# Performance work log

Hardware: AMD Instinct MI355X
Metric: run time of the kernel (lower is better)

## Reference

```python
import jax, jax.numpy as jnp
import numpy as np

B, S, D, H = 2, 2048, 2048, 16
HD = D // H  # 128 head dim


def setup_inputs() -> dict:
    key = jax.random.key(0)
    k1, k2, k3 = jax.random.split(key, 3)
    x = jax.random.normal(k1, (B, S, D), dtype=jnp.float32)
    w_qkv = jax.random.normal(k2, (3 * D, D), dtype=jnp.float32) * 0.02
    w_out = jax.random.normal(k3, (D, D), dtype=jnp.float32) * 0.02
    # complex-like RoPE table: freqs_cis[s, j] = exp(i * s * theta^{-2j/hd})
    theta = 10000.0
    inv_freq = 1.0 / (theta ** (jnp.arange(0, HD, 2, dtype=jnp.float32) / HD))  # [HD/2]
    t = jnp.arange(S, dtype=jnp.float32)
    freqs = jnp.outer(t, inv_freq)  # [S, HD/2]
    return {"x": x, "w_qkv": w_qkv, "w_out": w_out,
            "freqs_cos": jnp.cos(freqs), "freqs_sin": jnp.sin(freqs)}


def _apply_rope(t, cos, sin):
    # t: [b, s, h, hd]; adjacent pairs treated as complex (real, imag)
    b, s, h, hd = t.shape
    tr = t.reshape(b, s, h, hd // 2, 2)
    re, im = tr[..., 0], tr[..., 1]
    c = cos[None, :, None, :]  # [1, s, 1, hd/2]
    sn = sin[None, :, None, :]
    out_re = re * c - im * sn
    out_im = re * sn + im * c
    return jnp.stack([out_re, out_im], axis=-1).reshape(b, s, h, hd)


def reference(x, w_qkv, w_out, freqs_cos, freqs_sin):
    b, s, d = x.shape
    qkv = x @ w_qkv.T  # [b, s, 3d]
    q, k, v = jnp.split(qkv, 3, axis=-1)
    q = q.reshape(b, s, H, HD)
    k = k.reshape(b, s, H, HD)
    v = v.reshape(b, s, H, HD)
    q = _apply_rope(q, freqs_cos, freqs_sin)
    k = _apply_rope(k, freqs_cos, freqs_sin)
    # causal SDPA
    scale = 1.0 / jnp.sqrt(jnp.asarray(HD, dtype=x.dtype))
    scores = jnp.einsum("bqhd,bkhd->bhqk", q, k) * scale  # [b, h, s, s]
    causal = jnp.tril(jnp.ones((s, s), dtype=bool))
    scores = jnp.where(causal[None, None], scores, jnp.finfo(scores.dtype).min)
    attn = jax.nn.softmax(scores, axis=-1)
    out = jnp.einsum("bhqk,bkhd->bqhd", attn, v).reshape(b, s, d)
    return out @ w_out.T
```

## Files before the change

### kernel.cpp

```cpp
#include <hip/hip_runtime.h>
#include <hip/hip_bf16.h>
#include <stdint.h>

#define S_ 2048
#define D_ 2048
#define H_ 16
#define HD_ 128

typedef __bf16 bf16x8 __attribute__((ext_vector_type(8)));
typedef float f32x4 __attribute__((ext_vector_type(4)));
typedef unsigned short ushort_t;
typedef ushort_t us4 __attribute__((ext_vector_type(4)));

__device__ __forceinline__ float bf2f(ushort_t u) {
  union { float f; uint32_t i; } x; x.i = ((uint32_t)u) << 16; return x.f;
}
__device__ __forceinline__ ushort_t f2bf(float f) {
  union { float f; uint32_t i; } x; x.f = f;
  uint32_t r = x.i + 0x7fffu + ((x.i >> 16) & 1u);
  return (ushort_t)(r >> 16);
}

__device__ __forceinline__ void async_copy16(const void* g, void* l) {
  __builtin_amdgcn_global_load_lds(
      (const __attribute__((address_space(1))) unsigned int*)g,
      (__attribute__((address_space(3))) unsigned int*)l, 16, 0, 0);
}

__device__ __forceinline__ void store_val(float* p, float v) { *p = v; }
__device__ __forceinline__ void store_val(ushort_t* p, float v) { *p = f2bf(v); }

__global__ __launch_bounds__(256) void cvt_f32_bf16(const float* __restrict__ in,
                                                    ushort_t* __restrict__ out,
                                                    int n4) {
  int i = blockIdx.x * 256 + threadIdx.x;
  if (i >= n4) return;
  const float4 v = ((const float4*)in)[i];
  us4 o;
  o.x = f2bf(v.x); o.y = f2bf(v.y); o.z = f2bf(v.z); o.w = f2bf(v.w);
  ((us4*)out)[i] = o;
}

__device__ __forceinline__ void stage_half(const ushort_t* __restrict__ g, int K,
                                           ushort_t* l, int wave, int srow,
                                           int clog) {
#pragma unroll
  for (int i = 0; i < 2; ++i)
    async_copy16(g + (size_t)(i * 64 + srow) * K + clog * 8,
                 l + wave * 512 + i * 4096);
}

#define MFMA_BF16(a, b, c) __builtin_amdgcn_mfma_f32_16x16x32_bf16(a, b, c, 0, 0, 0)

template <typename OutT>
__global__ __launch_bounds__(512, 2) void gemm_bt128_256(const ushort_t* __restrict__ A,
                                                         const ushort_t* __restrict__ Bm,
                                                         OutT* __restrict__ C,
                                                         int M, int N, int K) {
  __shared__ __align__(16) ushort_t As[2][128 * 64];
  __shared__ __align__(16) ushort_t Bs[2][256 * 64];
  const int tid = threadIdx.x;
  const int wave = tid >> 6, lane = tid & 63;
  const int quad = lane >> 4, l16 = lane & 15;
  const int bm = blockIdx.y * 128, bn = blockIdx.x * 256;
  const int wm = (wave >> 2) * 64;
  const int wn = (wave & 3) * 64;
  const int srow = tid >> 3;
  const int clog = (tid & 7) ^ (srow & 7);
  const int ck0 = (quad ^ (l16 & 7)) * 8;
  const int ck1 = ((4 + quad) ^ (l16 & 7)) * 8;

  const ushort_t* gA = A + (size_t)bm * K;
  const ushort_t* gB = Bm + (size_t)bn * K;
  const int NT = K >> 6;

  f32x4 acc[4][4] = {};

  const ushort_t* ArowE = &As[0][0] + (wm + l16) * 64;
  const ushort_t* BrowE = &Bs[0][0] + (wn + l16) * 64;
  const ushort_t* ArowO = &As[1][0] + (wm + l16) * 64;
  const ushort_t* BrowO = &Bs[1][0] + (wn + l16) * 64;

  stage_half(gA, K, &As[0][0], wave, srow, clog);
  stage_half(gB, K, &Bs[0][0], wave, srow, clog);
  stage_half(gB + (size_t)128 * K, K, &Bs[0][8192], wave, srow, clog);
  stage_half(gB + 64, K, &Bs[1][0], wave, srow, clog);
  stage_half(gB + (size_t)128 * K + 64, K, &Bs[1][8192], wave, srow, clog);
  asm volatile("s_waitcnt vmcnt(4)" ::: "memory");
  __builtin_amdgcn_sched_barrier(0);
  __builtin_amdgcn_s_barrier();

  for (int ii = 0; ii < (NT >> 1); ++ii) {
    const int t = 2 * ii;
    const int t2 = (t + 2 < NT) ? t + 2 : NT - 1;
    const int t3 = (t + 3 < NT) ? t + 3 : NT - 1;
    const size_t k1 = (size_t)(t + 1) * 64;
    const size_t k2 = (size_t)t2 * 64;
    const size_t k3 = (size_t)t3 * 64;

    bf16x8 a4[4][2], b01[2][2], b23[2][2];

#pragma unroll
    for (int mi = 0; mi < 2; ++mi) {
      a4[mi][0] = *(const bf16x8*)(ArowE + mi * 1024 + ck0);
      a4[mi][1] = *(const bf16x8*)(ArowE + mi * 1024 + ck1);
    }
#pragma unroll
    for (int ni = 0; ni < 2; ++ni) {
      b01[ni][0] = *(const bf16x8*)(BrowE + ni * 1024 + ck0);
      b01[ni][1] = *(const bf16x8*)(BrowE + ni * 1024 + ck1);
    }
    stage_half(gA + k1, K, &As[1][0], wave, srow, clog);
    __builtin_amdgcn_s_barrier();
    __builtin_amdgcn_s_setprio(1);
#pragma unroll
    for (int ks = 0; ks < 2; ++ks)
#pragma unroll
      for (int mi = 0; mi < 2; ++mi)
#pragma unroll
        for (int ni = 0; ni < 2; ++ni)
          acc[mi][ni] = MFMA_BF16(a4[mi][ks], b01[ni][ks], acc[mi][ni]);
    __builtin_amdgcn_s_setprio(0);
    __builtin_amdgcn_s_barrier();

#pragma unroll
    for (int ni = 0; ni < 2; ++ni) {
      b23[ni][0] = *(const bf16x8*)(BrowE + (ni + 2) * 1024 + ck0);
      b23[ni][1] = *(const bf16x8*)(BrowE + (ni + 2) * 1024 + ck1);
    }
    __builtin_amdgcn_s_barrier();
    __builtin_amdgcn_s_setprio(1);
#pragma unroll
    for (int ks = 0; ks < 2; ++ks)
#pragma unroll
      for (int mi = 0; mi < 2; ++mi)
#pragma unroll
        for (int ni = 0; ni < 2; ++ni)
          acc[mi][ni + 2] = MFMA_BF16(a4[mi][ks], b23[ni][ks], acc[mi][ni + 2]);
    __builtin_amdgcn_s_setprio(0);
    __builtin_amdgcn_s_barrier();

#pragma unroll
    for (int mi = 0; mi < 2; ++mi) {
      a4[mi + 2][0] = *(const bf16x8*)(ArowE + (mi + 2) * 1024 + ck0);
      a4[mi + 2][1] = *(const bf16x8*)(ArowE + (mi + 2) * 1024 + ck1);
    }
    stage_half(gB + k2, K, &Bs[0][0], wave, srow, clog);
    __builtin_amdgcn_s_barrier();
    __builtin_amdgcn_s_setprio(1);
#pragma unroll
    for (int ks = 0; ks < 2; ++ks)
#pragma unroll
      for (int mi = 0; mi < 2; ++mi)
#pragma unroll
        for (int ni = 0; ni < 2; ++ni)
          acc[mi + 2][ni] = MFMA_BF16(a4[mi + 2][ks], b01[ni][ks], acc[mi + 2][ni]);
    __builtin_amdgcn_s_setprio(0);
    __builtin_amdgcn_s_barrier();

    stage_half(gB + (size_t)128 * K + k2, K, &Bs[0][8192], wave, srow, clog);
    asm volatile("s_waitcnt vmcnt(4)" ::: "memory");
    __builtin_amdgcn_sched_barrier(0);
    __builtin_amdgcn_s_barrier();
    __builtin_amdgcn_s_setprio(1);
#pragma unroll
    for (int ks = 0; ks < 2; ++ks)
#pragma unroll
      for (int mi = 0; mi < 2; ++mi)
#pragma unroll
        for (int ni = 0; ni < 2; ++ni)
          acc[mi + 2][ni + 2] = MFMA_BF16(a4[mi + 2][ks], b23[ni][ks], acc[mi + 2][ni + 2]);
    __builtin_amdgcn_s_setprio(0);
    __builtin_amdgcn_s_barrier();

#pragma unroll
    for (int mi = 0; mi < 2; ++mi) {
      a4[mi][0] = *(const bf16x8*)(ArowO + mi * 1024 + ck0);
      a4[mi][1] = *(const bf16x8*)(ArowO + mi * 1024 + ck1);
    }
#pragma unroll
    for (int ni = 0; ni < 2; ++ni) {
      b01[ni][0] = *(const bf16x8*)(BrowO + ni * 1024 + ck0);
      b01[ni][1] = *(const bf16x8*)(BrowO + ni * 1024 + ck1);
    }
    stage_half(gA + k2, K, &As[0][0], wave, srow, clog);
    __builtin_amdgcn_s_barrier();
    __builtin_amdgcn_s_setprio(1);
#pragma unroll
    for (int ks = 0; ks < 2; ++ks)
#pragma unroll
      for (int mi = 0; mi < 2; ++mi)
#pragma unroll
        for (int ni = 0; ni < 2; ++ni)
          acc[mi][ni] = MFMA_BF16(a4[mi][ks], b01[ni][ks], acc[mi][ni]);
    __builtin_amdgcn_s_setprio(0);
    __builtin_amdgcn_s_barrier();

#pragma unroll
    for (int ni = 0; ni < 2; ++ni) {
      b23[ni][0] = *(const bf16x8*)(BrowO + (ni + 2) * 1024 + ck0);
      b23[ni][1] = *(const bf16x8*)(BrowO + (ni + 2) * 1024 + ck1);
    }
    __builtin_amdgcn_s_barrier();
    __builtin_amdgcn_s_setprio(1);
#pragma unroll
    for (int ks = 0; ks < 2; ++ks)
#pragma unroll
      for (int mi = 0; mi < 2; ++mi)
#pragma unroll
        for (int ni = 0; ni < 2; ++ni)
          acc[mi][ni + 2] = MFMA_BF16(a4[mi][ks], b23[ni][ks], acc[mi][ni + 2]);
    __builtin_amdgcn_s_setprio(0);
    __builtin_amdgcn_s_barrier();

#pragma unroll
    for (int mi = 0; mi < 2; ++mi) {
      a4[mi + 2][0] = *(const bf16x8*)(ArowO + (mi + 2) * 1024 + ck0);
      a4[mi + 2][1] = *(const bf16x8*)(ArowO + (mi + 2) * 1024 + ck1);
    }
    stage_half(gB + k3, K, &Bs[1][0], wave, srow, clog);
    __builtin_amdgcn_s_barrier();
    __builtin_amdgcn_s_setprio(1);
#pragma unroll
    for (int ks = 0; ks < 2; ++ks)
#pragma unroll
      for (int mi = 0; mi < 2; ++mi)
#pragma unroll
        for (int ni = 0; ni < 2; ++ni)
          acc[mi + 2][ni] = MFMA_BF16(a4[mi + 2][ks], b01[ni][ks], acc[mi + 2][ni]);
    __builtin_amdgcn_s_setprio(0);
    __builtin_amdgcn_s_barrier();

    stage_half(gB + (size_t)128 * K + k3, K, &Bs[1][8192], wave, srow, clog);
    asm volatile("s_waitcnt vmcnt(4)" ::: "memory");
    __builtin_amdgcn_sched_barrier(0);
    __builtin_amdgcn_s_barrier();
    __builtin_amdgcn_s_setprio(1);
#pragma unroll
    for (int ks = 0; ks < 2; ++ks)
#pragma unroll
      for (int mi = 0; mi < 2; ++mi)
#pragma unroll
        for (int ni = 0; ni < 2; ++ni)
          acc[mi + 2][ni + 2] = MFMA_BF16(a4[mi + 2][ks], b23[ni][ks], acc[mi + 2][ni + 2]);
    __builtin_amdgcn_s_setprio(0);
    __builtin_amdgcn_s_barrier();
    __builtin_amdgcn_sched_barrier(0);
  }

  asm volatile("s_waitcnt vmcnt(0)" ::: "memory");

#pragma unroll
  for (int mi = 0; mi < 4; ++mi)
#pragma unroll
    for (int ni = 0; ni < 4; ++ni)
#pragma unroll
      for (int r = 0; r < 4; ++r) {
        int row = bm + wm + mi * 16 + quad * 4 + r;
        int col = bn + wn + ni * 16 + l16;
        store_val(&C[(size_t)row * N + col], acc[mi][ni][r]);
      }
}

__global__ __launch_bounds__(256) void rope_k(ushort_t* __restrict__ qkv,
                                              const float* __restrict__ fc,
                                              const float* __restrict__ fs) {
  int idx = blockIdx.x * 256 + threadIdx.x;
  int i = idx & 63;
  int hh = (idx >> 6) & 15;
  int m = idx >> 10;
  int s = m & (S_ - 1);
  float c = fc[s * 64 + i], sn = fs[s * 64 + i];
  size_t off = (size_t)m * (3 * D_) + hh * HD_ + 2 * i;
#pragma unroll
  for (int part = 0; part < 2; ++part) {
    uint32_t* p = (uint32_t*)(qkv + off + part * D_);
    uint32_t v = *p;
    float re = bf2f((ushort_t)(v & 0xffffu));
    float im = bf2f((ushort_t)(v >> 16));
    float nr = re * c - im * sn;
    float ni = re * sn + im * c;
    *p = (uint32_t)f2bf(nr) | ((uint32_t)f2bf(ni) << 16);
  }
}

__global__ __launch_bounds__(256) void vt_prep(const ushort_t* __restrict__ qkv,
                                               ushort_t* __restrict__ VTg) {
  __shared__ __align__(16) ushort_t T[64 * 136];
  const int st = blockIdx.x, h = blockIdx.y, b = blockIdx.z;
  const int tid = threadIdx.x;
  const ushort_t* gV = qkv + (size_t)(b * S_ + st * 64) * (3 * D_) + 2 * D_ + h * HD_;
  {
    const int r = tid >> 2, cc = (tid & 3) * 32;
    const ushort_t* src = gV + (size_t)r * (3 * D_) + cc;
    uint4 a0 = ((const uint4*)src)[0];
    uint4 a1 = ((const uint4*)src)[1];
    uint4 a2 = ((const uint4*)src)[2];
    uint4 a3 = ((const uint4*)src)[3];
    ushort_t* dst = T + r * 136 + cc;
    ((uint4*)dst)[0] = a0; ((uint4*)dst)[1] = a1;
    ((uint4*)dst)[2] = a2; ((uint4*)dst)[3] = a3;
  }
  __syncthreads();
  const int d = tid >> 1, kh = (tid & 1) * 32;
  ushort_t buf[32];
#pragma unroll
  for (int j = 0; j < 32; ++j) buf[j] = T[(kh + j) * 136 + d];
  ushort_t* out = VTg + ((size_t)((b * H_ + h) * HD_ + d)) * S_ + st * 64 + kh;
  ((uint4*)out)[0] = *(const uint4*)(buf + 0);
  ((uint4*)out)[1] = *(const uint4*)(buf + 8);
  ((uint4*)out)[2] = *(const uint4*)(buf + 16);
  ((uint4*)out)[3] = *(const uint4*)(buf + 24);
}

#define SOFTMAX_C 12.0f

__global__ __launch_bounds__(256, 4) void attn_fwd(const ushort_t* __restrict__ qkv,
                                                   const ushort_t* __restrict__ VTg,
                                                   float* __restrict__ Oacc,
                                                   float* __restrict__ lsum_g) {
  __shared__ __align__(16) ushort_t Kl[64 * 128];
  __shared__ __align__(16) ushort_t VT[128 * 64];
  __shared__ __align__(16) ushort_t Pl[4 * 16 * 64];

  const int j = 79 - (int)blockIdx.x;
  int qt, c;
  if (j < 8)       { qt = j;                 c = 0; }
  else if (j < 24) { int t = j - 8;  qt = 8 + (t >> 1);  c = t & 1; }
  else if (j < 48) { int t = j - 24; qt = 16 + t / 3;    c = t % 3; }
  else             { int t = j - 48; qt = 24 + (t >> 2); c = t & 3; }
  const int h = blockIdx.y, b = blockIdx.z;
  const int kt0 = c * 8;
  const int kt_end = min(kt0 + 8, qt + 1);

  const int tid = threadIdx.x;
  const int wave = tid >> 6, lane = tid & 63;
  const int quad = lane >> 4, l16 = lane & 15;
  const float scale = 0.08838834764831845f;

  const int qg = qt * 64 + wave * 16 + l16;
  const ushort_t* qrow = qkv + (size_t)(b * S_ + qg) * (3 * D_) + h * HD_;
  bf16x8 qf[4];
#pragma unroll
  for (int cc = 0; cc < 4; ++cc)
    qf[cc] = *(const bf16x8*)(qrow + cc * 32 + quad * 8);

  f32x4 o[8] = {};
  float lsum[4] = {0.f, 0.f, 0.f, 0.f};
  const int q_row_base = qt * 64 + wave * 16 + quad * 4;
  ushort_t* Pw = Pl + wave * 16 * 64;

  const ushort_t* gK = qkv + (size_t)(b * S_) * (3 * D_) + D_ + h * HD_;
  const ushort_t* gVT = VTg + (size_t)(b * H_ + h) * HD_ * S_;

  const int krow_off = lane >> 4;
  const int kchunk = lane & 15;
  const int vrow_off = lane >> 3;
  const int vchunk = lane & 7;

  for (int kt = kt0; kt < kt_end; ++kt) {
    __syncthreads();
#pragma unroll
    for (int i = 0; i < 4; ++i) {
      int row = wave * 16 + i * 4 + krow_off;
      int lchunk = kchunk ^ (row & 15);
      async_copy16(gK + (size_t)(kt * 64 + row) * (3 * D_) + lchunk * 8,
                   Kl + (wave * 16 + i * 4) * 128);
    }
#pragma unroll
    for (int i = 0; i < 4; ++i) {
      int row = wave * 32 + i * 8 + vrow_off;
      int lchunk = vchunk ^ (row & 7);
      async_copy16(gVT + (size_t)row * S_ + kt * 64 + lchunk * 8,
                   VT + (wave * 32 + i * 8) * 64);
    }
    __syncthreads();

    const bool diag = (kt == qt);
#pragma unroll
    for (int g = 0; g < 4; ++g) {
      f32x4 s = {0.f, 0.f, 0.f, 0.f};
#pragma unroll
      for (int cc = 0; cc < 4; ++cc) {
        bf16x8 kf = *(const bf16x8*)(Kl + (g * 16 + l16) * 128 +
                                     (((cc * 4 + quad) ^ l16) * 8));
        s = __builtin_amdgcn_mfma_f32_16x16x32_bf16(qf[cc], kf, s, 0, 0, 0);
      }
      const int key = kt * 64 + g * 16 + l16;
#pragma unroll
      for (int r = 0; r < 4; ++r) {
        float e = __expf(s[r] * scale - SOFTMAX_C);
        float p = (!diag || key <= q_row_base + r) ? e : 0.f;
        lsum[r] += p;
        int prow = quad * 4 + r;
        int pcol = g * 16 + l16;
        Pw[prow * 64 + (((pcol >> 3) ^ (prow & 7)) * 8) + (pcol & 7)] = f2bf(p);
      }
    }
    bf16x8 pf0 = *(const bf16x8*)(Pw + l16 * 64 + ((quad ^ (l16 & 7)) * 8));
    bf16x8 pf1 = *(const bf16x8*)(Pw + l16 * 64 + (((4 + quad) ^ (l16 & 7)) * 8));
#pragma unroll
    for (int dc = 0; dc < 8; ++dc) {
      bf16x8 v0 = *(const bf16x8*)(VT + (dc * 16 + l16) * 64 +
                                   (((0 * 4 + quad) ^ (l16 & 7)) * 8));
      o[dc] = __builtin_amdgcn_mfma_f32_16x16x32_bf16(pf0, v0, o[dc], 0, 0, 0);
      bf16x8 v1 = *(const bf16x8*)(VT + (dc * 16 + l16) * 64 +
                                   (((1 * 4 + quad) ^ (l16 & 7)) * 8));
      o[dc] = __builtin_amdgcn_mfma_f32_16x16x32_bf16(pf1, v1, o[dc], 0, 0, 0);
    }
  }

#pragma unroll
  for (int r = 0; r < 4; ++r) {
    float l = lsum[r];
    l += __shfl_xor(l, 1, 64);
    l += __shfl_xor(l, 2, 64);
    l += __shfl_xor(l, 4, 64);
    l += __shfl_xor(l, 8, 64);
    size_t row = (size_t)(b * S_ + q_row_base + r);
    if (l16 == 0) unsafeAtomicAdd(&lsum_g[row * H_ + h], l);
#pragma unroll
    for (int dc = 0; dc < 8; ++dc)
      unsafeAtomicAdd(&Oacc[row * D_ + h * HD_ + dc * 16 + l16], o[dc][r]);
  }
}

__global__ __launch_bounds__(256) void combine(const float* __restrict__ Oacc,
                                               const float* __restrict__ lsum_g,
                                               ushort_t* __restrict__ attn) {
  int i = blockIdx.x * 256 + threadIdx.x;
  float4 v = ((const float4*)Oacc)[i];
  int flat = i * 4;
  int row = flat >> 11;
  int h = (flat >> 7) & 15;
  float inv = 1.0f / lsum_g[row * H_ + h];
  us4 o;
  o.x = f2bf(v.x * inv); o.y = f2bf(v.y * inv);
  o.z = f2bf(v.z * inv); o.w = f2bf(v.w * inv);
  ((us4*)attn)[i] = o;
}

extern "C" void kernel_launch(void* const* d_in, const int* in_sizes, int n_in,
                              void* d_out, int out_size, void* d_ws, size_t ws_size,
                              hipStream_t stream) {
  const float* x = (const float*)d_in[0];
  const float* w_qkv = (const float*)d_in[1];
  const float* w_out = (const float*)d_in[2];
  const float* fcos = (const float*)d_in[3];
  const float* fsin = (const float*)d_in[4];
  float* out = (float*)d_out;

  char* ws = (char*)d_ws;
  ushort_t* x_bf    = (ushort_t*)(ws + 0);
  ushort_t* wqkv_bf = (ushort_t*)(ws + 16777216);
  ushort_t* wout_bf = (ushort_t*)(ws + 41943040);
  ushort_t* qkv     = (ushort_t*)(ws + 50331648);
  ushort_t* attn    = (ushort_t*)(ws + 100663296);
  float* Oacc   = (float*)(ws + 0);
  float* lsum_g = (float*)(ws + 33554432);
  ushort_t* VTg = (ushort_t*)(ws + 100663296);

  cvt_f32_bf16<<<8192, 256, 0, stream>>>(x, x_bf, 2097152);
  cvt_f32_bf16<<<12288, 256, 0, stream>>>(w_qkv, wqkv_bf, 3145728);
  cvt_f32_bf16<<<4096, 256, 0, stream>>>(w_out, wout_bf, 1048576);

  gemm_bt128_256<ushort_t><<<dim3(24, 32), 512, 0, stream>>>(x_bf, wqkv_bf, qkv,
                                                             4096, 6144, 2048);
  rope_k<<<16384, 256, 0, stream>>>(qkv, fcos, fsin);
  vt_prep<<<dim3(32, 16, 2), 256, 0, stream>>>(qkv, VTg);

  hipMemsetAsync(Oacc, 0, 33554432, stream);
  hipMemsetAsync(lsum_g, 0, 262144, stream);

  attn_fwd<<<dim3(80, 16, 2), 256, 0, stream>>>(qkv, VTg, Oacc, lsum_g);
  combine<<<8192, 256, 0, stream>>>(Oacc, lsum_g, attn);

  gemm_bt128_256<float><<<dim3(8, 32), 512, 0, stream>>>(attn, wout_bf, out,
                                                         4096, 2048, 2048);
}
```

Before: 446.2 us.

## Add higher-occupancy QKV GEMM with 32-wide K tiles and triple-buffered B

Adds a new GEMM kernel for the QKV projection that uses 32-element K tiles, two A buffers and three rotating B buffers, cutting LDS use so that more blocks fit per CU (launch bounds 512,4). The main loop is split into half-steps that interleave async global-to-LDS staging with MFMA groups, using barriers and setprio to overlap loads with compute. Smaller K tiles mean more barriers per unit of work and a different swizzle, which could offset the latency-hiding gain from the extra occupancy. The output-projection GEMM still uses the old kernel.

```diff
diff --git a/kernel.cpp b/kernel.cpp
--- a/kernel.cpp
+++ b/kernel.cpp
@@ -41,6 +41,154 @@
   ((us4*)out)[i] = o;
 }
 
+__device__ __forceinline__ void stage_B32(const ushort_t* __restrict__ g, int K,
+                                          ushort_t* l, int wave, int srow,
+                                          int clog) {
+  async_copy16(g + (size_t)srow * K + clog * 8, l + wave * 512);
+  async_copy16(g + (size_t)(128 + srow) * K + clog * 8, l + 4096 + wave * 512);
+}
+__device__ __forceinline__ void stage_A32(const ushort_t* __restrict__ g, int K,
+                                          ushort_t* l, int wave, int srow,
+                                          int clog) {
+  async_copy16(g + (size_t)srow * K + clog * 8, l + wave * 512);
+}
+
+#define MFMA_BF16(a, b, c) __builtin_amdgcn_mfma_f32_16x16x32_bf16(a, b, c, 0, 0, 0)
+
+template <typename OutT>
+__global__ __launch_bounds__(512, 4) void gemm_bt_occ2(const ushort_t* __restrict__ A,
+                                                       const ushort_t* __restrict__ Bm,
+                                                       OutT* __restrict__ C,
+                                                       int M, int N, int K) {
+  __shared__ __align__(16) ushort_t As[2][128 * 32];
+  __shared__ __align__(16) ushort_t Bs[3][256 * 32];
+  const int tid = threadIdx.x;
+  const int wave = tid >> 6, lane = tid & 63;
+  const int quad = lane >> 4, l16 = lane & 15;
+  const int bm = blockIdx.y * 128, bn = blockIdx.x * 256;
+  const int wm = (wave >> 2) * 64;
+  const int wn = (wave & 3) * 64;
+  const int srow = tid >> 2;
+  const int clog = (tid & 3) ^ ((tid >> 3) & 3);
+  const int ck = (quad ^ ((l16 >> 1) & 3)) * 8;
+
+  const ushort_t* gA = A + (size_t)bm * K;
+  const ushort_t* gB = Bm + (size_t)bn * K;
+  const int NT = K >> 5;
+
+  f32x4 acc[4][4] = {};
+
+  const int arow0 = (wm + l16) * 32 + ck;
+  const int brow0 = (wn + l16) * 32 + ck;
+
+  stage_B32(gB, K, &Bs[0][0], wave, srow, clog);
+  stage_A32(gA, K, &As[0][0], wave, srow, clog);
+  stage_B32(gB + 32, K, &Bs[1][0], wave, srow, clog);
+  stage_A32(gA + 32, K, &As[1][0], wave, srow, clog);
+  asm volatile("s_waitcnt vmcnt(3)" ::: "memory");
+  __builtin_amdgcn_sched_barrier(0);
+  __builtin_amdgcn_s_barrier();
+
+  int bc = 0;
+  for (int ii = 0; ii < (NT >> 1); ++ii) {
+    const int t = 2 * ii;
+    const size_t k2 = (size_t)((t + 2 < NT) ? t + 2 : NT - 1) * 32;
+    const size_t k3 = (size_t)((t + 3 < NT) ? t + 3 : NT - 1) * 32;
+    const int bc1 = (bc + 1 < 3) ? bc + 1 : 0;
+    const int bc2 = (bc + 2 < 3) ? bc + 2 : bc - 1;
+    const ushort_t* At = &As[0][0];
+    const ushort_t* At1 = &As[1][0];
+    const ushort_t* Bt = &Bs[0][0] + bc * 8192;
+    const ushort_t* Bt1 = &Bs[0][0] + bc1 * 8192;
+    ushort_t* Bw2 = &Bs[0][0] + bc2 * 8192;
+    ushort_t* Bw0 = &Bs[0][0] + bc * 8192;
+
+    bf16x8 a4[4], b0[2], b1[2];
+
+#pragma unroll
+    for (int mi = 0; mi < 4; ++mi)
+      a4[mi] = *(const bf16x8*)(At + arow0 + mi * 512);
+#pragma unroll
+    for (int ni = 0; ni < 2; ++ni)
+      b0[ni] = *(const bf16x8*)(Bt + brow0 + ni * 512);
+    stage_B32(gB + k2, K, Bw2, wave, srow, clog);
+    __builtin_amdgcn_s_barrier();
+    __builtin_amdgcn_s_setprio(1);
+#pragma unroll
+    for (int mi = 0; mi < 4; ++mi)
+#pragma unroll
+      for (int ni = 0; ni < 2; ++ni)
+        acc[mi][ni] = MFMA_BF16(a4[mi], b0[ni], acc[mi][ni]);
+    __builtin_amdgcn_s_setprio(0);
+    __builtin_amdgcn_s_barrier();
+
+#pragma unroll
+    for (int ni = 0; ni < 2; ++ni)
+      b1[ni] = *(const bf16x8*)(Bt + brow0 + (ni + 2) * 512);
+    stage_A32(gA + k2, K, &As[0][0], wave, srow, clog);
+    asm volatile("s_waitcnt vmcnt(3)" ::: "memory");
+    __builtin_amdgcn_sched_barrier(0);
+    __builtin_amdgcn_s_barrier();
+    __builtin_amdgcn_s_setprio(1);
+#pragma unroll
+    for (int mi = 0; mi < 4; ++mi)
+#pragma unroll
+      for (int ni = 0; ni < 2; ++ni)
+        acc[mi][ni + 2] = MFMA_BF16(a4[mi], b1[ni], acc[mi][ni + 2]);
+    __builtin_amdgcn_s_setprio(0);
+    __builtin_amdgcn_s_barrier();
+
+#pragma unroll
+    for (int mi = 0; mi < 4; ++mi)
+      a4[mi] = *(const bf16x8*)(At1 + arow0 + mi * 512);
+#pragma unroll
+    for (int ni = 0; ni < 2; ++ni)
+      b0[ni] = *(const bf16x8*)(Bt1 + brow0 + ni * 512);
+    stage_B32(gB + k3, K, Bw0, wave, srow, clog);
+    __builtin_amdgcn_s_barrier();
+    __builtin_amdgcn_s_setprio(1);
+#pragma unroll
+    for (int mi = 0; mi < 4; ++mi)
+#pragma unroll
+      for (int ni = 0; ni < 2; ++ni)
+        acc[mi][ni] = MFMA_BF16(a4[mi], b0[ni], acc[mi][ni]);
+    __builtin_amdgcn_s_setprio(0);
+    __builtin_amdgcn_s_barrier();
+
+#pragma unroll
+    for (int ni = 0; ni < 2; ++ni)
+      b1[ni] = *(const bf16x8*)(Bt1 + brow0 + (ni + 2) * 512);
+    stage_A32(gA + k3, K, &As[1][0], wave, srow, clog);
+    asm volatile("s_waitcnt vmcnt(3)" ::: "memory");
+    __builtin_amdgcn_sched_barrier(0);
+    __builtin_amdgcn_s_barrier();
+    __builtin_amdgcn_s_setprio(1);
+#pragma unroll
+    for (int mi = 0; mi < 4; ++mi)
+#pragma unroll
+      for (int ni = 0; ni < 2; ++ni)
+        acc[mi][ni + 2] = MFMA_BF16(a4[mi], b1[ni], acc[mi][ni + 2]);
+    __builtin_amdgcn_s_setprio(0);
+    __builtin_amdgcn_s_barrier();
+    __builtin_amdgcn_sched_barrier(0);
+
+    bc = bc2;
+  }
+
+  asm volatile("s_waitcnt vmcnt(0)" ::: "memory");
+
+#pragma unroll
+  for (int mi = 0; mi < 4; ++mi)
+#pragma unroll
+    for (int ni = 0; ni < 4; ++ni)
+#pragma unroll
+      for (int r = 0; r < 4; ++r) {
+        int row = bm + wm + mi * 16 + quad * 4 + r;
+        int col = bn + wn + ni * 16 + l16;
+        store_val(&C[(size_t)row * N + col], acc[mi][ni][r]);
+      }
+}
+
 __device__ __forceinline__ void stage_half(const ushort_t* __restrict__ g, int K,
                                            ushort_t* l, int wave, int srow,
                                            int clog) {
@@ -49,8 +197,6 @@
     async_copy16(g + (size_t)(i * 64 + srow) * K + clog * 8,
                  l + wave * 512 + i * 4096);
 }
-
-#define MFMA_BF16(a, b, c) __builtin_amdgcn_mfma_f32_16x16x32_bf16(a, b, c, 0, 0, 0)
 
 template <typename OutT>
 __global__ __launch_bounds__(512, 2) void gemm_bt128_256(const ushort_t* __restrict__ A,
@@ -464,13 +610,13 @@
   cvt_f32_bf16<<<12288, 256, 0, stream>>>(w_qkv, wqkv_bf, 3145728);
   cvt_f32_bf16<<<4096, 256, 0, stream>>>(w_out, wout_bf, 1048576);
 
-  gemm_bt128_256<ushort_t><<<dim3(24, 32), 512, 0, stream>>>(x_bf, wqkv_bf, qkv,
-                                                             4096, 6144, 2048);
+  gemm_bt_occ2<ushort_t><<<dim3(24, 32), 512, 0, stream>>>(x_bf, wqkv_bf, qkv,
+                                                           4096, 6144, 2048);
   rope_k<<<16384, 256, 0, stream>>>(qkv, fcos, fsin);
   vt_prep<<<dim3(32, 16, 2), 256, 0, stream>>>(qkv, VTg);
 
-  hipMemsetAsync(Oacc, 0, 33554432, stream);
-  hipMemsetAsync(lsum_g, 0, 262144, stream);
+  (void)hipMemsetAsync(Oacc, 0, 33554432, stream);
+  (void)hipMemsetAsync(lsum_g, 0, 262144, stream);
 
   attn_fwd<<<dim3(80, 16, 2), 256, 0, stream>>>(qkv, VTg, Oacc, lsum_g);
   combine<<<8192, 256, 0, stream>>>(Oacc, lsum_g, attn);
```

After: 446.0 us. Within noise of the previous version (-0.0%).
